# Performance work log

Measured on AMD Instinct MI355X. Metric: run time of the kernel, lower is better.

## Reference

```python
import jax, jax.numpy as jnp
import numpy as np

B, S, D, H = 2, 2048, 1024, 16

def setup_inputs() -> dict:
    key = jax.random.key(0)
    k_x, k_wq, k_bq, k_wk, k_wv = jax.random.split(key, 5)
    return {
        "x": jax.random.normal(k_x, (B, S, D), dtype=jnp.float32),
        "Wq": jax.random.normal(k_wq, (D, D), dtype=jnp.float32) / 100.0,
        "Bq": jax.random.normal(k_bq, (1, D), dtype=jnp.float32) / 100.0,
        "Wk": jax.random.normal(k_wk, (D, D), dtype=jnp.float32) / 100.0,
        "Wv": jax.random.normal(k_wv, (D, D), dtype=jnp.float32) / 100.0,
        "n_heads": H,
    }

def reference(x, Wq, Bq, Wk, Wv, n_heads):
    b, s, d = x.shape
    dh = d // n_heads
    # Projections
    Q = x @ Wq + Bq          # [b, s, d]
    K = x @ Wk               # [b, s, d]
    V = x @ Wv               # [b, s, d]
    # Unconventional head split: last dim -> (d_head, n_heads), heads LAST
    Q = Q.reshape(b, s, dh, n_heads)
    K = K.reshape(b, s, dh, n_heads)
    V = V.reshape(b, s, dh, n_heads)
    # NOTE: original scales by sqrt(d_model), not sqrt(d_head)
    scale = 1.0 / np.sqrt(d).astype(np.float32)
    scores = jnp.einsum('bidh,bjdh->bijh', Q, K) * scale  # [b, i, j, h]
    attn = jax.nn.softmax(scores, axis=2)                 # softmax over j
    out = jnp.einsum('bijh,bjdh->bidh', attn, V)          # [b, i, dh, h]
    return out.reshape(b, s, d)                            # merge_heads
```

## Files before the change

### kernel.cpp

```cpp
#include <hip/hip_runtime.h>

#define B_ 2
#define S_ 2048
#define D_ 1024
#define H_ 16

typedef __attribute__((ext_vector_type(8))) short short8;
typedef __attribute__((ext_vector_type(8))) unsigned short ushort8;
typedef __attribute__((ext_vector_type(4))) short short4v;
typedef __attribute__((ext_vector_type(4))) float f32x4;

__device__ __forceinline__ unsigned short f2b(float f){
  unsigned u = __float_as_uint(f);
  u += 0x7fffu + ((u >> 16) & 1u);
  return (unsigned short)(u >> 16);
}
__device__ __forceinline__ float b2f(unsigned short b){
  return __uint_as_float(((unsigned)b) << 16);
}
__device__ __forceinline__ float fast_exp2(float x){
#if __has_builtin(__builtin_amdgcn_exp2f)
  return __builtin_amdgcn_exp2f(x);
#else
  return exp2f(x);
#endif
}
__device__ __forceinline__ unsigned pack_trunc(unsigned u_lo, unsigned u_hi){
#if __has_builtin(__builtin_amdgcn_perm)
  return __builtin_amdgcn_perm(u_hi, u_lo, 0x07060302u);
#else
  return (u_lo >> 16) | (u_hi & 0xffff0000u);
#endif
}
__device__ __forceinline__ f32x4 mfma16(short8 a, short8 b, f32x4 c){
  return __builtin_amdgcn_mfma_f32_16x16x32_bf16(a, b, c, 0, 0, 0);
}
__device__ __forceinline__ void gload_lds16(const void* g, void* l){
  __builtin_amdgcn_global_load_lds((const __attribute__((address_space(1))) unsigned int*)g,
                                   (__attribute__((address_space(3))) unsigned int*)l, 16, 0, 0);
}

__global__ __launch_bounds__(256) void prep(const float* __restrict__ x,
                                            const float* __restrict__ Wq,
                                            const float* __restrict__ Wk,
                                            const float* __restrict__ Wv,
                                            unsigned short* __restrict__ xbf,
                                            unsigned short* __restrict__ wT){
  const int z = blockIdx.z;
  if (z == 3){
    int lb = blockIdx.y * 32 + blockIdx.x;
    int i = (lb * 256 + threadIdx.x) * 16;
    #pragma unroll
    for (int half = 0; half < 2; half++){
      f32x4 a = *(const f32x4*)(x + i + half * 8);
      f32x4 b = *(const f32x4*)(x + i + half * 8 + 4);
      ushort8 o;
      o[0]=f2b(a[0]); o[1]=f2b(a[1]); o[2]=f2b(a[2]); o[3]=f2b(a[3]);
      o[4]=f2b(b[0]); o[5]=f2b(b[1]); o[6]=f2b(b[2]); o[7]=f2b(b[3]);
      *(ushort8*)(xbf + i + half * 8) = o;
    }
    return;
  }
  const float* W = (z == 0) ? Wq : ((z == 1) ? Wk : Wv);
  __shared__ float tile[32][33];
  int nb = blockIdx.x * 32, kb = blockIdx.y * 32;
  int tx = threadIdx.x & 31, ty = threadIdx.x >> 5;
  #pragma unroll
  for (int it = 0; it < 4; it++){
    int row = ty + it * 8;
    tile[row][tx] = W[(size_t)(kb + row) * D_ + nb + tx];
  }
  __syncthreads();
  unsigned short* outp = wT + (size_t)z * D_ * D_;
  #pragma unroll
  for (int it = 0; it < 4; it++){
    int row = ty + it * 8;
    int n = nb + row;
    int np = ((n & 15) << 6) | (n >> 4);
    outp[(size_t)np * D_ + kb + tx] = f2b(tile[tx][row]);
  }
}

__global__ __launch_bounds__(256) void qkv_gemm(const unsigned short* __restrict__ xbf,
                                                const unsigned short* __restrict__ wT,
                                                const float* __restrict__ Bq,
                                                unsigned short* __restrict__ qatt,
                                                unsigned short* __restrict__ katt,
                                                unsigned short* __restrict__ vatt){
  __shared__ char SM[34816];
  unsigned short* Ct = (unsigned short*)SM;
  const int proj = blockIdx.z;
  const int mbase = blockIdx.y * 128, nbase = blockIdx.x * 128;
  const unsigned short* bsrc = wT + (size_t)proj * D_ * D_;
  const int t = threadIdx.x, w = t >> 6, lane = t & 63, ln = lane & 15, hi = lane >> 4;
  const int wr = w >> 1, wc = w & 1;
  const int srow = t >> 2, scol = (t & 3) << 3;
  f32x4 acc[4][4] = {};

  #pragma unroll
  for (int i = 0; i < 2; i++){
    gload_lds16(xbf  + (size_t)(mbase + srow + i * 64) * D_ + scol, SM + w * 1024 + i * 4096);
    gload_lds16(bsrc + (size_t)(nbase + srow + i * 64) * D_ + scol, SM + 8192 + w * 1024 + i * 4096);
  }
  __syncthreads();

  int cur = 0;
  for (int ks = 0; ks < D_; ks += 32){
    if (ks + 32 < D_){
      char* nb_ = SM + (cur ^ 1) * 16384;
      #pragma unroll
      for (int i = 0; i < 2; i++){
        gload_lds16(xbf  + (size_t)(mbase + srow + i * 64) * D_ + ks + 32 + scol, nb_ + w * 1024 + i * 4096);
        gload_lds16(bsrc + (size_t)(nbase + srow + i * 64) * D_ + ks + 32 + scol, nb_ + 8192 + w * 1024 + i * 4096);
      }
    }
    const unsigned short* At = (const unsigned short*)(SM + cur * 16384);
    const unsigned short* Bt = (const unsigned short*)(SM + cur * 16384 + 8192);
    short8 af[4], bf[4];
    #pragma unroll
    for (int q = 0; q < 4; q++) af[q] = *(const short8*)&At[(wr * 64 + q * 16 + ln) * 32 + hi * 8];
    #pragma unroll
    for (int p = 0; p < 4; p++) bf[p] = *(const short8*)&Bt[(wc * 64 + p * 16 + ln) * 32 + hi * 8];
    #pragma unroll
    for (int q = 0; q < 4; q++)
      #pragma unroll
      for (int p = 0; p < 4; p++)
        acc[q][p] = mfma16(af[q], bf[p], acc[q][p]);
    __syncthreads();
    cur ^= 1;
  }

  const float qscale = 0.04508422002778011f;
  const int b = mbase >> 11, ms = mbase & 2047;

  if (proj == 2){
    #pragma unroll
    for (int p = 0; p < 4; p++)
      #pragma unroll
      for (int q = 0; q < 4; q++)
        #pragma unroll
        for (int r = 0; r < 4; r++)
          Ct[(wc*64 + p*16 + ln) * 136 + wr*64 + q*16 + hi*4 + r] = f2b(acc[q][p][r]);
    __syncthreads();
    #pragma unroll
    for (int j = 0; j < 8; j++){
      int u = j * 256 + t;
      int col = u >> 4, s0 = (u & 15) * 8;
      int h = blockIdx.x * 2 + (col >> 6), r = col & 63;
      short8 v = *(const short8*)&Ct[col * 136 + s0];
      *(short8*)&vatt[((size_t)(b*16 + h) * 64 + r) * 2048 + ms + s0] = v;
    }
  } else {
    const int hglob = blockIdx.x * 2 + wc;
    #pragma unroll
    for (int p = 0; p < 4; p++){
      float bqv = (proj == 0) ? Bq[(p*16 + ln)*16 + hglob] : 0.f;
      #pragma unroll
      for (int q = 0; q < 4; q++)
        #pragma unroll
        for (int r = 0; r < 4; r++){
          float v = acc[q][p][r];
          if (proj == 0) v = (v + bqv) * qscale;
          Ct[(wr*64 + q*16 + hi*4 + r) * 136 + wc*64 + p*16 + ln] = f2b(v);
        }
    }
    __syncthreads();
    unsigned short* dstb = (proj == 0) ? qatt : katt;
    #pragma unroll
    for (int j = 0; j < 8; j++){
      int u = j * 256 + t;
      int hl = u >> 10, rem = u & 1023, sl = rem >> 3, r0 = (rem & 7) * 8;
      int h = blockIdx.x * 2 + hl;
      short8 v = *(const short8*)&Ct[sl * 136 + hl*64 + r0];
      *(short8*)&dstb[((size_t)(b*16 + h) * 2048 + ms + sl) * 64 + r0] = v;
    }
  }
}

template<int NS>
__global__ __launch_bounds__(256) void attn_fwd(const unsigned short* __restrict__ qatt,
                                                const unsigned short* __restrict__ katt,
                                                const unsigned short* __restrict__ vatt,
                                                unsigned short* __restrict__ pnum,
                                                float* __restrict__ pden){
  __shared__ unsigned short Kt[2][64 * 64];
  __shared__ unsigned short Vt[2][64 * 64];
  const int t = threadIdx.x, w = t >> 6, lane = t & 63, ln = lane & 15, hi = lane >> 4;
  const int bid = blockIdx.x;
  const int bpx = (512 * NS) / 8;
  const int L = (bid & 7) * bpx + (bid >> 3);
  const int bh = L / (16 * NS);
  const int rem = L % (16 * NS);
  const int z = rem >> 4, qc = rem & 15;
  const int b = bh >> 4, h = bh & 15;
  const int q0 = qc * 128 + w * 32;
  const int kvbase = z * (S_ / NS);
  const int NT = (S_ / NS) / 64;
  const unsigned short* Qh = qatt + (size_t)bh * S_ * 64;
  const unsigned short* Kh = katt + (size_t)bh * S_ * 64;
  const unsigned short* Vh = vatt + (size_t)bh * 64 * S_;

  short8 qf[2][2];
  #pragma unroll
  for (int qb = 0; qb < 2; qb++)
    #pragma unroll
    for (int kc = 0; kc < 2; kc++)
      qf[qb][kc] = *(const short8*)&Qh[(size_t)(q0 + qb * 16 + ln) * 64 + kc * 32 + hi * 8];

  const int srow = w * 16 + (lane >> 3);
  const int scol0 = ((lane & 7) * 16) ^ ((srow & 7) << 4);
  const int scol1 = ((lane & 7) * 16) ^ (((srow + 8) & 7) << 4);
  const int t0 = srow, t1 = srow + 8;
  const int kp0 = ((t0 >> 5) << 5) | (((t0 >> 2) & 3) << 3) | (((t0 >> 4) & 1) << 2) | (t0 & 3);
  const int kp1 = ((t1 >> 5) << 5) | (((t1 >> 2) & 3) << 3) | (((t1 >> 4) & 1) << 2) | (t1 & 3);

  f32x4 acc[2][4] = {};
  f32x4 accd[2] = {};
  const short8 vones8 = {(short)0x3F80, (short)0x3F80, (short)0x3F80, (short)0x3F80,
                         (short)0x3F80, (short)0x3F80, (short)0x3F80, (short)0x3F80};

  {
    int kv = kvbase;
    gload_lds16(Kh + (size_t)(kv + kp0) * 64 + (scol0 >> 1), (char*)&Kt[0][0] + w * 2048);
    gload_lds16(Kh + (size_t)(kv + kp1) * 64 + (scol1 >> 1), (char*)&Kt[0][0] + w * 2048 + 1024);
    gload_lds16(Vh + (size_t)srow * S_ + kv + (scol0 >> 1),       (char*)&Vt[0][0] + w * 2048);
    gload_lds16(Vh + (size_t)(srow + 8) * S_ + kv + (scol1 >> 1), (char*)&Vt[0][0] + w * 2048 + 1024);
  }
  __syncthreads();

  int cur = 0;
  for (int tt = 0; tt < NT; ++tt){
    if (tt + 1 < NT){
      int kv = kvbase + (tt + 1) * 64;
      int nb = cur ^ 1;
      gload_lds16(Kh + (size_t)(kv + kp0) * 64 + (scol0 >> 1), (char*)&Kt[nb][0] + w * 2048);
      gload_lds16(Kh + (size_t)(kv + kp1) * 64 + (scol1 >> 1), (char*)&Kt[nb][0] + w * 2048 + 1024);
      gload_lds16(Vh + (size_t)srow * S_ + kv + (scol0 >> 1),       (char*)&Vt[nb][0] + w * 2048);
      gload_lds16(Vh + (size_t)(srow + 8) * S_ + kv + (scol1 >> 1), (char*)&Vt[nb][0] + w * 2048 + 1024);
    }
    const unsigned short* Kc = &Kt[cur][0];
    const unsigned short* Vc = &Vt[cur][0];

    short8 kf[4][2];
    #pragma unroll
    for (int kb = 0; kb < 4; kb++)
      #pragma unroll
      for (int kc = 0; kc < 2; kc++){
        int eb = (((kc * 64 + hi * 16) ^ ((ln & 7) << 4)) >> 1);
        kf[kb][kc] = *(const short8*)&Kc[(kb * 16 + ln) * 64 + eb];
      }

    short8 pa8[2][2];
    #pragma unroll
    for (int qb = 0; qb < 2; qb++)
      #pragma unroll
      for (int W = 0; W < 2; W++){
        f32x4 za = {0.f, 0.f, 0.f, 0.f};
        za = mfma16(kf[2*W][0], qf[qb][0], za);
        za = mfma16(kf[2*W][1], qf[qb][1], za);
        f32x4 zb = {0.f, 0.f, 0.f, 0.f};
        zb = mfma16(kf[2*W+1][0], qf[qb][0], zb);
        zb = mfma16(kf[2*W+1][1], qf[qb][1], zb);
        unsigned a0 = __float_as_uint(fast_exp2(za[0]));
        unsigned a1 = __float_as_uint(fast_exp2(za[1]));
        unsigned a2 = __float_as_uint(fast_exp2(za[2]));
        unsigned a3 = __float_as_uint(fast_exp2(za[3]));
        unsigned b0 = __float_as_uint(fast_exp2(zb[0]));
        unsigned b1 = __float_as_uint(fast_exp2(zb[1]));
        unsigned b2 = __float_as_uint(fast_exp2(zb[2]));
        unsigned b3 = __float_as_uint(fast_exp2(zb[3]));
        union { unsigned u[4]; short8 s; } pk;
        pk.u[0] = pack_trunc(a0, a1);
        pk.u[1] = pack_trunc(a2, a3);
        pk.u[2] = pack_trunc(b0, b1);
        pk.u[3] = pack_trunc(b2, b3);
        pa8[qb][W] = pk.s;
        accd[qb] = mfma16(pa8[qb][W], vones8, accd[qb]);
      }

    #pragma unroll
    for (int cb = 0; cb < 4; cb++)
      #pragma unroll
      for (int W = 0; W < 2; W++){
        int eb = (((W * 64 + hi * 16) ^ ((ln & 7) << 4)) >> 1);
        short8 vf = *(const short8*)&Vc[(cb * 16 + ln) * 64 + eb];
        acc[0][cb] = mfma16(pa8[0][W], vf, acc[0][cb]);
        acc[1][cb] = mfma16(pa8[1][W], vf, acc[1][cb]);
      }
    __syncthreads();
    cur ^= 1;
  }

  if (ln == 0){
    #pragma unroll
    for (int qb = 0; qb < 2; qb++)
      #pragma unroll
      for (int r = 0; r < 4; r++)
        pden[((size_t)(z * 2 + b) * S_ + q0 + qb * 16 + hi * 4 + r) * 16 + h] = accd[qb][r];
  }

  const size_t rowb = (size_t)(z * 2 + b) * S_;
  #pragma unroll
  for (int qb = 0; qb < 2; qb++)
    #pragma unroll
    for (int cb = 0; cb < 4; cb++)
      #pragma unroll
      for (int r = 0; r < 4; r++){
        int qrow = q0 + qb * 16 + hi * 4 + r;
        pnum[(rowb + qrow) * 1024 + h * 64 + cb * 16 + ln] = f2b(acc[qb][cb][r]);
      }
}

template<int NSPLIT>
__global__ __launch_bounds__(256) void attn_reduce(const unsigned short* __restrict__ pnum,
                                                   const float* __restrict__ pden,
                                                   float* __restrict__ out){
  __shared__ float L[4 * 1056];
  const int t = threadIdx.x;
  const int row_l = t >> 6, lane = t & 63;
  const int grow = blockIdx.x * 4 + row_l;
  const int e0 = lane * 16;
  const int h = e0 >> 6;
  float den = 0.f;
  float nsum[16];
  #pragma unroll
  for (int j = 0; j < 16; j++) nsum[j] = 0.f;
  #pragma unroll
  for (int z = 0; z < NSPLIT; z++){
    const size_t prow = (size_t)z * 4096 + grow;
    den += pden[prow * 16 + h];
    #pragma unroll
    for (int c = 0; c < 2; c++){
      ushort8 nv = *(const ushort8*)&pnum[prow * 1024 + e0 + c * 8];
      #pragma unroll
      for (int k = 0; k < 8; k++) nsum[c*8 + k] += b2f(nv[k]);
    }
  }
  float rinv = 1.0f / den;
  #pragma unroll
  for (int j = 0; j < 16; j++){
    int col = e0 + j;
    L[row_l * 1056 + col + (col >> 5)] = nsum[j] * rinv;
  }
  __syncthreads();
  const int d0 = lane * 16;
  #pragma unroll
  for (int c = 0; c < 4; c++){
    f32x4 o;
    #pragma unroll
    for (int k = 0; k < 4; k++){
      int d = d0 + c * 4 + k;
      int e = ((d & 15) << 6) | (d >> 4);
      o[k] = L[row_l * 1056 + e + (e >> 5)];
    }
    *(f32x4*)&out[(size_t)grow * 1024 + d0 + c * 4] = o;
  }
}

extern "C" void kernel_launch(void* const* d_in, const int* in_sizes, int n_in,
                              void* d_out, int out_size, void* d_ws, size_t ws_size,
                              hipStream_t stream){
  const float* x  = (const float*)d_in[0];
  const float* Wq = (const float*)d_in[1];
  const float* Bq = (const float*)d_in[2];
  const float* Wk = (const float*)d_in[3];
  const float* Wv = (const float*)d_in[4];
  char* ws = (char*)d_ws;
  const size_t MB = 1024 * 1024;
  unsigned short* qatt = (unsigned short*)(ws);
  unsigned short* katt = (unsigned short*)(ws + 8 * MB);
  unsigned short* vatt = (unsigned short*)(ws + 16 * MB);
  unsigned short* xbf  = (unsigned short*)(ws + 24 * MB);
  unsigned short* wT   = (unsigned short*)(ws + 32 * MB);
  float* outp = (float*)d_out;

  prep<<<dim3(32, 32, 4), 256, 0, stream>>>(x, Wq, Wk, Wv, xbf, wT);
  qkv_gemm<<<dim3(8, 32, 3), 256, 0, stream>>>(xbf, wT, Bq, qatt, katt, vatt);

  if (ws_size >= 59 * MB){
    const int NS = 4;
    unsigned short* pnum = (unsigned short*)(ws + 24 * MB);
    float* pden = (float*)(ws + 24 * MB + (size_t)NS * 8 * MB);
    attn_fwd<NS><<<512 * NS, 256, 0, stream>>>(qatt, katt, vatt, pnum, pden);
    attn_reduce<NS><<<1024, 256, 0, stream>>>(pnum, pden, outp);
  } else if (ws_size >= 42 * MB){
    const int NS = 2;
    unsigned short* pnum = (unsigned short*)(ws + 24 * MB);
    float* pden = (float*)(ws + 24 * MB + (size_t)NS * 8 * MB);
    attn_fwd<NS><<<512 * NS, 256, 0, stream>>>(qatt, katt, vatt, pnum, pden);
    attn_reduce<NS><<<1024, 256, 0, stream>>>(pnum, pden, outp);
  } else {
    const int NS = 1;
    unsigned short* pnum = (unsigned short*)(ws + 24 * MB);
    float* pden = (float*)(ws + 24 * MB + (size_t)NS * 8 * MB);
    attn_fwd<NS><<<512 * NS, 256, 0, stream>>>(qatt, katt, vatt, pnum, pden);
    attn_reduce<NS><<<1024, 256, 0, stream>>>(pnum, pden, outp);
  }
}
```

Before: 100.00 us.

## Replace double-buffered K/V LDS tiles with single buffer and priority boosting

Drops the double-buffered K/V shared-memory tiles in the attention kernel in favour of a single buffer. Each iteration now loads its own tile, synchronises, computes, and synchronises again, and the compute section runs at raised wave priority via s_setprio. The intent is to halve LDS use so more blocks fit per CU and cross-block overlap hides load latency instead of in-block prefetch. The risk is that within a block the load latency is exposed every iteration, and there are two barriers per tile instead of one.

```diff
diff --git a/kernel.cpp b/kernel.cpp
--- a/kernel.cpp
+++ b/kernel.cpp
@@ -183,8 +183,8 @@
                                                 const unsigned short* __restrict__ vatt,
                                                 unsigned short* __restrict__ pnum,
                                                 float* __restrict__ pden){
-  __shared__ unsigned short Kt[2][64 * 64];
-  __shared__ unsigned short Vt[2][64 * 64];
+  __shared__ unsigned short Kt[64 * 64];
+  __shared__ unsigned short Vt[64 * 64];
   const int t = threadIdx.x, w = t >> 6, lane = t & 63, ln = lane & 15, hi = lane >> 4;
   const int bid = blockIdx.x;
   const int bpx = (512 * NS) / 8;
@@ -219,35 +219,22 @@
   const short8 vones8 = {(short)0x3F80, (short)0x3F80, (short)0x3F80, (short)0x3F80,
                          (short)0x3F80, (short)0x3F80, (short)0x3F80, (short)0x3F80};
 
-  {
-    int kv = kvbase;
-    gload_lds16(Kh + (size_t)(kv + kp0) * 64 + (scol0 >> 1), (char*)&Kt[0][0] + w * 2048);
-    gload_lds16(Kh + (size_t)(kv + kp1) * 64 + (scol1 >> 1), (char*)&Kt[0][0] + w * 2048 + 1024);
-    gload_lds16(Vh + (size_t)srow * S_ + kv + (scol0 >> 1),       (char*)&Vt[0][0] + w * 2048);
-    gload_lds16(Vh + (size_t)(srow + 8) * S_ + kv + (scol1 >> 1), (char*)&Vt[0][0] + w * 2048 + 1024);
-  }
-  __syncthreads();
-
-  int cur = 0;
   for (int tt = 0; tt < NT; ++tt){
-    if (tt + 1 < NT){
-      int kv = kvbase + (tt + 1) * 64;
-      int nb = cur ^ 1;
-      gload_lds16(Kh + (size_t)(kv + kp0) * 64 + (scol0 >> 1), (char*)&Kt[nb][0] + w * 2048);
-      gload_lds16(Kh + (size_t)(kv + kp1) * 64 + (scol1 >> 1), (char*)&Kt[nb][0] + w * 2048 + 1024);
-      gload_lds16(Vh + (size_t)srow * S_ + kv + (scol0 >> 1),       (char*)&Vt[nb][0] + w * 2048);
-      gload_lds16(Vh + (size_t)(srow + 8) * S_ + kv + (scol1 >> 1), (char*)&Vt[nb][0] + w * 2048 + 1024);
-    }
-    const unsigned short* Kc = &Kt[cur][0];
-    const unsigned short* Vc = &Vt[cur][0];
-
+    const int kv = kvbase + tt * 64;
+    gload_lds16(Kh + (size_t)(kv + kp0) * 64 + (scol0 >> 1), (char*)Kt + w * 2048);
+    gload_lds16(Kh + (size_t)(kv + kp1) * 64 + (scol1 >> 1), (char*)Kt + w * 2048 + 1024);
+    gload_lds16(Vh + (size_t)srow * S_ + kv + (scol0 >> 1),       (char*)Vt + w * 2048);
+    gload_lds16(Vh + (size_t)(srow + 8) * S_ + kv + (scol1 >> 1), (char*)Vt + w * 2048 + 1024);
+    __syncthreads();
+
+    __builtin_amdgcn_s_setprio(1);
     short8 kf[4][2];
     #pragma unroll
     for (int kb = 0; kb < 4; kb++)
       #pragma unroll
       for (int kc = 0; kc < 2; kc++){
         int eb = (((kc * 64 + hi * 16) ^ ((ln & 7) << 4)) >> 1);
-        kf[kb][kc] = *(const short8*)&Kc[(kb * 16 + ln) * 64 + eb];
+        kf[kb][kc] = *(const short8*)&Kt[(kb * 16 + ln) * 64 + eb];
       }
 
     short8 pa8[2][2];
@@ -283,12 +270,12 @@
       #pragma unroll
       for (int W = 0; W < 2; W++){
         int eb = (((W * 64 + hi * 16) ^ ((ln & 7) << 4)) >> 1);
-        short8 vf = *(const short8*)&Vc[(cb * 16 + ln) * 64 + eb];
+        short8 vf = *(const short8*)&Vt[(cb * 16 + ln) * 64 + eb];
         acc[0][cb] = mfma16(pa8[0][W], vf, acc[0][cb]);
         acc[1][cb] = mfma16(pa8[1][W], vf, acc[1][cb]);
       }
-    __syncthreads();
-    cur ^= 1;
+    __builtin_amdgcn_s_setprio(0);
+    __syncthreads();
   }
 
   if (ln == 0){
```

New measurement: 97.64 us, median of 2. -2.4%, faster.
